# Optimization experiments

Measured on AMD Instinct MI355X. Metric: run time of the kernel, lower is better.

The kernel has to match this reference:

```python
import jax, jax.numpy as jnp
import numpy as np

N_GRAPHS = 1024   # pool of learnable adjacency blocks (len(Adjs))
BLOCK = 128       # nodes per graph (block size)
BATCH = 1024      # len(batch_idrange); D = BATCH * BLOCK rows
FEAT = 32         # input feature dim


def setup_inputs() -> dict:
    key = jax.random.key(0)
    k1, k2, k3 = jax.random.split(key, 3)
    # learnable per-graph adjacency weights (self.weights stacked)
    weights = jax.random.normal(k1, (N_GRAPHS, BLOCK, BLOCK), dtype=jnp.float32)
    # dense node-feature input [D, F] with D = BATCH * BLOCK
    inp = jax.random.normal(k2, (BATCH * BLOCK, FEAT), dtype=jnp.float32)
    # which adjacency block each batch element uses
    batch_idrange = jax.random.randint(k3, (BATCH,), 0, N_GRAPHS, dtype=jnp.int64)
    return {"input": inp, "weights": weights, "batch_idrange": batch_idrange}


def reference(input, weights, batch_idrange):
    # Original: blockdiag(weights[batch_idrange]) @ input.
    # Block-diagonal structure means each block only touches its own row slab,
    # so this is exactly a batched per-block matmul (same math, no zero padding).
    B = batch_idrange.shape[0]
    n = weights.shape[1]
    W = weights[batch_idrange]                    # [B, n, n] gather (irregular access)
    xb = input.reshape(B, n, -1)                  # [B, n, F]
    out = jnp.einsum('bij,bjf->bif', W, xb)       # [B, n, F]
    return out.reshape(input.shape[0], -1)        # [D, F]
```

## Files before the change

kernel.cpp:

```cpp
#include <hip/hip_runtime.h>

#define NODES 128
#define FEAT  32
#define XPAD  136

typedef __attribute__((ext_vector_type(8))) short bf16x8;
typedef __attribute__((ext_vector_type(4))) float f32x4;

__device__ __forceinline__ unsigned pk_bf16(float a, float b) {
    unsigned ua = __builtin_bit_cast(unsigned, a);
    unsigned ub = __builtin_bit_cast(unsigned, b);
    ua += 0x7fffu + ((ua >> 16) & 1u);
    ub += 0x7fffu + ((ub >> 16) & 1u);
    return (ua >> 16) | (ub & 0xffff0000u);
}

__device__ __forceinline__ bf16x8 cvt_frag(float4 lo, float4 hi) {
    union { unsigned u[4]; bf16x8 v; } r;
    r.u[0] = pk_bf16(lo.x, lo.y);
    r.u[1] = pk_bf16(lo.z, lo.w);
    r.u[2] = pk_bf16(hi.x, hi.y);
    r.u[3] = pk_bf16(hi.z, hi.w);
    return r.v;
}

__global__ __launch_bounds__(512, 6)
void blockdiag_mm(const float* __restrict__ inp,
                  const float* __restrict__ weights,
                  const int* __restrict__ idx,
                  float* __restrict__ out)
{
    __shared__ __align__(16) short xt[FEAT * XPAD];

    const int b  = blockIdx.x;
    const int u  = threadIdx.x;
    const int w  = u >> 6;
    const int l  = u & 63;
    const int ln = l & 15;
    const int q  = l >> 4;

    const float* __restrict__ xin = inp + (size_t)b * (NODES * FEAT);
    const float* __restrict__ wb  = weights + (size_t)idx[b] * (NODES * NODES);

    const float4* x4 = (const float4*)xin;
    const int fq = u & 7;
    const int k0 = (u >> 3) * 2;
    const float4 v0 = x4[k0 * 8 + fq];
    const float4 v1 = x4[(k0 + 1) * 8 + fq];

    const float4* w4 = (const float4*)wb;
    const int wbase = (16 * w + ln) * 32 + q * 2;
    float4 wf[8];
    #pragma unroll
    for (int kb = 0; kb < 4; ++kb) {
        wf[2 * kb + 0] = w4[wbase + kb * 8 + 0];
        wf[2 * kb + 1] = w4[wbase + kb * 8 + 1];
    }

    {
        const float pv0[4] = {v0.x, v0.y, v0.z, v0.w};
        const float pv1[4] = {v1.x, v1.y, v1.z, v1.w};
        #pragma unroll
        for (int i = 0; i < 4; ++i)
            *(unsigned*)(&xt[(fq * 4 + i) * XPAD + k0]) = pk_bf16(pv0[i], pv1[i]);
    }

    __builtin_amdgcn_sched_barrier(0);
    asm volatile("s_waitcnt lgkmcnt(0)" ::: "memory");
    __builtin_amdgcn_s_barrier();
    __builtin_amdgcn_sched_barrier(0);

    f32x4 acc[2] = {};
    #pragma unroll
    for (int kb = 0; kb < 4; ++kb) {
        const bf16x8 afr = cvt_frag(wf[2 * kb + 0], wf[2 * kb + 1]);
        #pragma unroll
        for (int nt = 0; nt < 2; ++nt) {
            const bf16x8 bfr = *(const bf16x8*)(&xt[(16 * nt + ln) * XPAD + kb * 32 + q * 8]);
            acc[nt] = __builtin_amdgcn_mfma_f32_16x16x32_bf16(afr, bfr, acc[nt], 0, 0, 0);
        }
    }

    float* ob = out + (size_t)b * (NODES * FEAT);
    #pragma unroll
    for (int nt = 0; nt < 2; ++nt)
        #pragma unroll
        for (int reg = 0; reg < 4; ++reg)
            ob[(16 * w + q * 4 + reg) * FEAT + 16 * nt + ln] = acc[nt][reg];
}

extern "C" void kernel_launch(void* const* d_in, const int* in_sizes, int n_in,
                              void* d_out, int out_size, void* d_ws, size_t ws_size,
                              hipStream_t stream) {
    const float* inp = (const float*)d_in[0];
    const float* wts = (const float*)d_in[1];
    const int*   idx = (const int*)d_in[2];
    float* outp = (float*)d_out;
    const int B = in_sizes[2];
    hipLaunchKernelGGL(blockdiag_mm, dim3(B), dim3(512), 0, stream,
                       inp, wts, idx, outp);
}
```

Measured before the change: 111.2 us.

## Process two batch elements per workgroup to raise memory-level parallelism

Each workgroup now handles two adjacent batch elements. It issues both weight-block gathers and both input loads up front, then runs the MFMA loops for each element and writes both outputs. The grid is halved and launch bounds drop from 6 to 4 waves per SIMD. The goal is to overlap more outstanding global loads per thread and amortise launch and barrier overhead, at the cost of more registers, double the LDS per block, and fewer workgroups to spread across CUs.

```diff
diff --git a/kernel.cpp b/kernel.cpp
--- a/kernel.cpp
+++ b/kernel.cpp
@@ -24,45 +24,59 @@
     return r.v;
 }
 
-__global__ __launch_bounds__(512, 6)
+__global__ __launch_bounds__(512, 4)
 void blockdiag_mm(const float* __restrict__ inp,
                   const float* __restrict__ weights,
                   const int* __restrict__ idx,
-                  float* __restrict__ out)
+                  float* __restrict__ out,
+                  int B)
 {
-    __shared__ __align__(16) short xt[FEAT * XPAD];
+    __shared__ __align__(16) short xt[2][FEAT * XPAD];
 
-    const int b  = blockIdx.x;
+    const int b0 = 2 * blockIdx.x;
+    const int b1 = b0 + 1;
+    const bool b1ok = (b1 < B);
+
     const int u  = threadIdx.x;
     const int w  = u >> 6;
     const int l  = u & 63;
     const int ln = l & 15;
     const int q  = l >> 4;
 
-    const float* __restrict__ xin = inp + (size_t)b * (NODES * FEAT);
-    const float* __restrict__ wb  = weights + (size_t)idx[b] * (NODES * NODES);
+    const int i0 = idx[b0];
+    const int i1 = b1ok ? idx[b1] : i0;
 
-    const float4* x4 = (const float4*)xin;
+    const float4* x40 = (const float4*)(inp + (size_t)b0 * (NODES * FEAT));
+    const float4* x41 = x40 + (NODES * FEAT / 4);
     const int fq = u & 7;
     const int k0 = (u >> 3) * 2;
-    const float4 v0 = x4[k0 * 8 + fq];
-    const float4 v1 = x4[(k0 + 1) * 8 + fq];
+    float4 xv[4];
+    xv[0] = x40[k0 * 8 + fq];
+    xv[1] = x40[(k0 + 1) * 8 + fq];
+    xv[2] = x41[k0 * 8 + fq];
+    xv[3] = x41[(k0 + 1) * 8 + fq];
 
-    const float4* w4 = (const float4*)wb;
+    const float4* w4e[2] = {
+        (const float4*)(weights + (size_t)i0 * (NODES * NODES)),
+        (const float4*)(weights + (size_t)i1 * (NODES * NODES))
+    };
     const int wbase = (16 * w + ln) * 32 + q * 2;
-    float4 wf[8];
+    float4 wf[2][8];
     #pragma unroll
-    for (int kb = 0; kb < 4; ++kb) {
-        wf[2 * kb + 0] = w4[wbase + kb * 8 + 0];
-        wf[2 * kb + 1] = w4[wbase + kb * 8 + 1];
-    }
+    for (int e = 0; e < 2; ++e)
+        #pragma unroll
+        for (int kb = 0; kb < 4; ++kb) {
+            wf[e][2 * kb + 0] = w4e[e][wbase + kb * 8 + 0];
+            wf[e][2 * kb + 1] = w4e[e][wbase + kb * 8 + 1];
+        }
 
-    {
-        const float pv0[4] = {v0.x, v0.y, v0.z, v0.w};
-        const float pv1[4] = {v1.x, v1.y, v1.z, v1.w};
+    #pragma unroll
+    for (int e = 0; e < 2; ++e) {
+        const float pv0[4] = {xv[2*e].x, xv[2*e].y, xv[2*e].z, xv[2*e].w};
+        const float pv1[4] = {xv[2*e+1].x, xv[2*e+1].y, xv[2*e+1].z, xv[2*e+1].w};
         #pragma unroll
         for (int i = 0; i < 4; ++i)
-            *(unsigned*)(&xt[(fq * 4 + i) * XPAD + k0]) = pk_bf16(pv0[i], pv1[i]);
+            *(unsigned*)(&xt[e][(fq * 4 + i) * XPAD + k0]) = pk_bf16(pv0[i], pv1[i]);
     }
 
     __builtin_amdgcn_sched_barrier(0);
@@ -70,23 +84,27 @@
     __builtin_amdgcn_s_barrier();
     __builtin_amdgcn_sched_barrier(0);
 
-    f32x4 acc[2] = {};
     #pragma unroll
-    for (int kb = 0; kb < 4; ++kb) {
-        const bf16x8 afr = cvt_frag(wf[2 * kb + 0], wf[2 * kb + 1]);
+    for (int e = 0; e < 2; ++e) {
+        f32x4 acc[2] = {};
         #pragma unroll
-        for (int nt = 0; nt < 2; ++nt) {
-            const bf16x8 bfr = *(const bf16x8*)(&xt[(16 * nt + ln) * XPAD + kb * 32 + q * 8]);
-            acc[nt] = __builtin_amdgcn_mfma_f32_16x16x32_bf16(afr, bfr, acc[nt], 0, 0, 0);
+        for (int kb = 0; kb < 4; ++kb) {
+            const bf16x8 afr = cvt_frag(wf[e][2 * kb + 0], wf[e][2 * kb + 1]);
+            #pragma unroll
+            for (int nt = 0; nt < 2; ++nt) {
+                const bf16x8 bfr = *(const bf16x8*)(&xt[e][(16 * nt + ln) * XPAD + kb * 32 + q * 8]);
+                acc[nt] = __builtin_amdgcn_mfma_f32_16x16x32_bf16(afr, bfr, acc[nt], 0, 0, 0);
+            }
+        }
+        if (e == 0 || b1ok) {
+            float* ob = out + (size_t)(b0 + e) * (NODES * FEAT);
+            #pragma unroll
+            for (int nt = 0; nt < 2; ++nt)
+                #pragma unroll
+                for (int reg = 0; reg < 4; ++reg)
+                    ob[(16 * w + q * 4 + reg) * FEAT + 16 * nt + ln] = acc[nt][reg];
         }
     }
-
-    float* ob = out + (size_t)b * (NODES * FEAT);
-    #pragma unroll
-    for (int nt = 0; nt < 2; ++nt)
-        #pragma unroll
-        for (int reg = 0; reg < 4; ++reg)
-            ob[(16 * w + q * 4 + reg) * FEAT + 16 * nt + ln] = acc[nt][reg];
 }
 
 extern "C" void kernel_launch(void* const* d_in, const int* in_sizes, int n_in,
@@ -97,6 +115,6 @@
     const int*   idx = (const int*)d_in[2];
     float* outp = (float*)d_out;
     const int B = in_sizes[2];
-    hipLaunchKernelGGL(blockdiag_mm, dim3(B), dim3(512), 0, stream,
-                       inp, wts, idx, outp);
+    hipLaunchKernelGGL(blockdiag_mm, dim3((B + 1) / 2), dim3(512), 0, stream,
+                       inp, wts, idx, outp, B);
 }
```

Result: no change. 109.9 us (-1.2%).
